# Kernel optimization log

Hardware: AMD Instinct MI355X
Metric: run time of the kernel (lower is better)

## Reference

```python
import jax, jax.numpy as jnp
import numpy as np

M, IN, H, OUT, B = 64, 64, 256, 1, 4096


def setup_inputs() -> dict:
    key = jax.random.key(0)
    ks = jax.random.split(key, 7)
    s1 = 1.0 / np.sqrt(IN)
    s2 = 1.0 / np.sqrt(H)
    return {
        "xs": jax.random.normal(ks[0], (M, B, IN), dtype=jnp.float32),
        "W1": jax.random.uniform(ks[1], (M, IN, H), minval=-s1, maxval=s1, dtype=jnp.float32),
        "b1": jax.random.uniform(ks[2], (M, H), minval=-s1, maxval=s1, dtype=jnp.float32),
        "W2": jax.random.uniform(ks[3], (M, H, H), minval=-s2, maxval=s2, dtype=jnp.float32),
        "b2": jax.random.uniform(ks[4], (M, H), minval=-s2, maxval=s2, dtype=jnp.float32),
        "W3": jax.random.uniform(ks[5], (M, H, OUT), minval=-s2, maxval=s2, dtype=jnp.float32),
        "b3": jax.random.uniform(ks[6], (M, OUT), minval=-s2, maxval=s2, dtype=jnp.float32),
    }


def reference(xs, W1, b1, W2, b2, W3, b3):
    # Batched over models: [M, B, in] x [M, in, h] -> [M, B, h]
    h1 = jax.nn.relu(jnp.einsum("mbi,mih->mbh", xs, W1) + b1[:, None, :])
    h2 = jax.nn.relu(jnp.einsum("mbh,mhk->mbk", h1, W2) + b2[:, None, :])
    out = jnp.einsum("mbh,mho->mbo", h2, W3) + b3[:, None, :]
    return out  # [M, B, out]
```

## Files before the change

### kernel.cpp

```cpp
#include <hip/hip_runtime.h>
#include <hip/hip_bf16.h>

#define NMODELS 64
#define BBATCH  4096
#define IN_DIM  64
#define H_DIM   256

typedef __attribute__((ext_vector_type(8))) short short8;
typedef __attribute__((ext_vector_type(4))) float floatx4;
typedef __attribute__((ext_vector_type(4))) unsigned int uint4v;
typedef __attribute__((ext_vector_type(2))) unsigned int uint2v;

__device__ __forceinline__ unsigned short f2bf(float f) {
    unsigned int u = __builtin_bit_cast(unsigned int, f);
    return (unsigned short)((u + 0x8000u) >> 16);
}
__device__ __forceinline__ unsigned int pkbf(float a, float b) {
    __hip_bfloat162 h = __float22bfloat162_rn(make_float2(a, b));
    unsigned int u;
    __builtin_memcpy(&u, &h, 4);
    return u;
}

__global__ __launch_bounds__(256) void prep_weights(const float* __restrict__ W1,
                                                    const float* __restrict__ W2,
                                                    unsigned short* __restrict__ w1t,
                                                    unsigned short* __restrict__ w2t) {
    __shared__ float lds[64][65];
    const int bid = blockIdx.x;
    const float* src;
    unsigned short* dst;
    int K, N, m, kb, nb;
    if (bid < 256) {
        m = bid >> 2; kb = 0; nb = bid & 3; K = IN_DIM; N = H_DIM;
        src = W1; dst = w1t;
    } else {
        int t = bid - 256;
        m = t >> 4; kb = (t >> 2) & 3; nb = t & 3; K = H_DIM; N = H_DIM;
        src = W2; dst = w2t;
    }
    const float* s = src + ((size_t)m * K + (size_t)kb * 64) * N + nb * 64;
    const int tid = threadIdx.x;
    const int r = tid >> 4, c4 = (tid & 15) * 4;
#pragma unroll
    for (int p = 0; p < 4; ++p) {
        int row = p * 16 + r;
        float4 v = *(const float4*)(s + (size_t)row * N + c4);
        lds[row][c4] = v.x; lds[row][c4 + 1] = v.y;
        lds[row][c4 + 2] = v.z; lds[row][c4 + 3] = v.w;
    }
    __syncthreads();
    unsigned short* dbase = dst + ((size_t)m * N + (size_t)nb * 64) * K + kb * 64;
    const int j = tid & 7;
#pragma unroll
    for (int it = 0; it < 2; ++it) {
        int n = it * 32 + (tid >> 3);
        unsigned short tmp[8];
#pragma unroll
        for (int e = 0; e < 8; ++e) tmp[e] = f2bf(lds[j * 8 + e][n]);
        *(short8*)(dbase + (size_t)n * K + j * 8) = *(const short8*)tmp;
    }
}

__global__ __launch_bounds__(256, 2) void mlp_fused(
    const float* __restrict__ xs,
    const unsigned short* __restrict__ w1t,
    const float* __restrict__ b1,
    const unsigned short* __restrict__ w2t,
    const float* __restrict__ b2,
    const float* __restrict__ w3,
    const float* __restrict__ b3,
    float* __restrict__ out)
{
    __shared__ unsigned short h1s[2][64 * 256];
    float* red = (float*)h1s;

    const int bid = blockIdx.x;
    const int m     = bid >> 5;
    const int tile0 = (bid & 31) * 2;
    const int tid = threadIdx.x;
    const int w   = tid >> 6;
    const int lane = tid & 63;
    const int q   = lane >> 4;
    const int c16 = lane & 15;
    const int sw  = c16 & 7;

    floatx4 b1v = *(const floatx4*)(b1 + m * H_DIM + w * 64 + c16 * 4);
    floatx4 b2v = *(const floatx4*)(b2 + m * H_DIM + w * 64 + c16 * 4);
    floatx4 w3v = *(const floatx4*)(w3 + m * H_DIM + w * 64 + c16 * 4);
    const float b3v = b3[m];

    const float* xrow0 = xs + ((size_t)m * BBATCH + (size_t)tile0 * 64) * IN_DIM;
    const unsigned short* w1p = w1t + (size_t)m * (H_DIM * IN_DIM)
                                + (w * 64 + c16 * 4) * IN_DIM + q * 8;
    const unsigned short* w2p = w2t + (size_t)m * (H_DIM * H_DIM)
                                + (w * 64 + c16 * 4) * H_DIM + q * 8;

    short8 ax[2][4][2];
#pragma unroll
    for (int t = 0; t < 2; ++t)
#pragma unroll
        for (int rb = 0; rb < 4; ++rb)
#pragma unroll
            for (int kb = 0; kb < 2; ++kb) {
                const float* xp = xrow0 + (size_t)t * 64 * IN_DIM
                                  + (rb * 16 + c16) * IN_DIM + kb * 32 + q * 8;
                float4 v0 = *(const float4*)xp;
                float4 v1 = *(const float4*)(xp + 4);
                uint4v u;
                u[0] = pkbf(v0.x, v0.y); u[1] = pkbf(v0.z, v0.w);
                u[2] = pkbf(v1.x, v1.y); u[3] = pkbf(v1.z, v1.w);
                ax[t][rb][kb] = __builtin_bit_cast(short8, u);
            }

    floatx4 acc[2][4][4];
#pragma unroll
    for (int t = 0; t < 2; ++t)
#pragma unroll
        for (int rb = 0; rb < 4; ++rb)
#pragma unroll
            for (int nb = 0; nb < 4; ++nb)
                acc[t][rb][nb] = (floatx4){0.f, 0.f, 0.f, 0.f};

    {
        short8 bw[2][4];
#pragma unroll
        for (int kb = 0; kb < 2; ++kb)
#pragma unroll
            for (int nb = 0; nb < 4; ++nb)
                bw[kb][nb] = *(const short8*)(w1p + nb * IN_DIM + kb * 32);
#pragma unroll
        for (int t = 0; t < 2; ++t)
#pragma unroll
            for (int kb = 0; kb < 2; ++kb)
#pragma unroll
                for (int nb = 0; nb < 4; ++nb)
#pragma unroll
                    for (int rb = 0; rb < 4; ++rb)
                        acc[t][rb][nb] = __builtin_amdgcn_mfma_f32_16x16x32_bf16(
                            ax[t][rb][kb], bw[kb][nb], acc[t][rb][nb], 0, 0, 0);
    }

    short8 bv[3][4];
#pragma unroll
    for (int nb = 0; nb < 4; ++nb) bv[0][nb] = *(const short8*)(w2p + nb * H_DIM + 0 * 32);
#pragma unroll
    for (int nb = 0; nb < 4; ++nb) bv[1][nb] = *(const short8*)(w2p + nb * H_DIM + 1 * 32);

    {
#pragma unroll
        for (int t = 0; t < 2; ++t)
#pragma unroll
            for (int rb = 0; rb < 4; ++rb)
#pragma unroll
                for (int r = 0; r < 4; ++r) {
                    float v0 = fmaxf(acc[t][rb][0][r] + b1v[0], 0.f);
                    float v1 = fmaxf(acc[t][rb][1][r] + b1v[1], 0.f);
                    float v2 = fmaxf(acc[t][rb][2][r] + b1v[2], 0.f);
                    float v3 = fmaxf(acc[t][rb][3][r] + b1v[3], 0.f);
                    uint2v u; u[0] = pkbf(v0, v1); u[1] = pkbf(v2, v3);
                    int row = rb * 16 + q * 4 + r;
                    int chunk = (w * 8 + (c16 >> 1)) ^ (row & 7);
                    *(uint2v*)((char*)&h1s[t][0] + row * 512 + chunk * 16 + (c16 & 1) * 8) = u;
                }
    }
    __syncthreads();

#pragma unroll
    for (int t = 0; t < 2; ++t)
#pragma unroll
        for (int rb = 0; rb < 4; ++rb)
#pragma unroll
            for (int nb = 0; nb < 4; ++nb)
                acc[t][rb][nb] = (floatx4){0.f, 0.f, 0.f, 0.f};

#pragma unroll
    for (int kb = 0; kb < 8; ++kb) {
        const int cur = kb % 3;
        const int pre = (kb + 2) % 3;
        if (kb < 6) {
#pragma unroll
            for (int nb = 0; nb < 4; ++nb)
                bv[pre][nb] = *(const short8*)(w2p + nb * H_DIM + (kb + 2) * 32);
        }
        short8 av[2][4];
#pragma unroll
        for (int t = 0; t < 2; ++t)
#pragma unroll
            for (int rb = 0; rb < 4; ++rb)
                av[t][rb] = *(const short8*)((char*)&h1s[t][0] + (rb * 16 + c16) * 512
                                             + (((kb * 4 + q) ^ sw) * 16));
#pragma unroll
        for (int nb = 0; nb < 4; ++nb)
#pragma unroll
            for (int t = 0; t < 2; ++t)
#pragma unroll
                for (int rb = 0; rb < 4; ++rb)
                    acc[t][rb][nb] = __builtin_amdgcn_mfma_f32_16x16x32_bf16(
                        av[t][rb], bv[cur][nb], acc[t][rb][nb], 0, 0, 0);
    }

    float p[2][4][4];
#pragma unroll
    for (int t = 0; t < 2; ++t)
#pragma unroll
        for (int rb = 0; rb < 4; ++rb)
#pragma unroll
            for (int r = 0; r < 4; ++r) p[t][rb][r] = 0.f;
#pragma unroll
    for (int t = 0; t < 2; ++t)
#pragma unroll
        for (int rb = 0; rb < 4; ++rb)
#pragma unroll
            for (int nb = 0; nb < 4; ++nb)
#pragma unroll
                for (int r = 0; r < 4; ++r) {
                    float v = fmaxf(acc[t][rb][nb][r] + b2v[nb], 0.f);
                    p[t][rb][r] += v * w3v[nb];
                }
#pragma unroll
    for (int off = 1; off < 16; off <<= 1)
#pragma unroll
        for (int t = 0; t < 2; ++t)
#pragma unroll
            for (int rb = 0; rb < 4; ++rb)
#pragma unroll
                for (int r = 0; r < 4; ++r)
                    p[t][rb][r] += __shfl_xor(p[t][rb][r], off);

    __syncthreads();
    if (c16 == 0) {
#pragma unroll
        for (int t = 0; t < 2; ++t)
#pragma unroll
            for (int rb = 0; rb < 4; ++rb)
#pragma unroll
                for (int r = 0; r < 4; ++r)
                    red[t * 256 + w * 64 + rb * 16 + q * 4 + r] = p[t][rb][r];
    }
    __syncthreads();
    if (tid < 128) {
        int t = tid >> 6, rr = tid & 63;
        const float* rt = red + t * 256;
        float s = rt[rr] + rt[64 + rr] + rt[128 + rr] + rt[192 + rr] + b3v;
        out[(size_t)m * BBATCH + (tile0 + t) * 64 + rr] = s;
    }
}

extern "C" void kernel_launch(void* const* d_in, const int* in_sizes, int n_in,
                              void* d_out, int out_size, void* d_ws, size_t ws_size,
                              hipStream_t stream) {
    const float* xs = (const float*)d_in[0];
    const float* W1 = (const float*)d_in[1];
    const float* b1 = (const float*)d_in[2];
    const float* W2 = (const float*)d_in[3];
    const float* b2 = (const float*)d_in[4];
    const float* W3 = (const float*)d_in[5];
    const float* b3 = (const float*)d_in[6];
    float* out = (float*)d_out;

    unsigned short* w1t = (unsigned short*)d_ws;
    unsigned short* w2t = w1t + (size_t)NMODELS * H_DIM * IN_DIM;

    prep_weights<<<256 + NMODELS * 16, 256, 0, stream>>>(W1, W2, w1t, w2t);
    mlp_fused<<<NMODELS * (BBATCH / 128), 256, 0, stream>>>(xs, w1t, b1, w2t, b2, W3, b3, out);
}
```

Measured before the change: 181.2 us.

## Process one 64-row tile per block to raise occupancy

Each block now handles a single 64-row batch tile instead of two. This halves the LDS buffer, the accumulator registers and the A-fragment registers, so launch bounds can ask for three blocks per CU and the grid doubles. The W2 prefetch pipeline also shrinks from triple to double buffering. The trade-off is that each W2 fragment loaded from global or L2 is reused across half as many rows, which doubles weight traffic per output.

```diff
diff --git a/kernel.cpp b/kernel.cpp
--- a/kernel.cpp
+++ b/kernel.cpp
@@ -62,7 +62,7 @@
     }
 }
 
-__global__ __launch_bounds__(256, 2) void mlp_fused(
+__global__ __launch_bounds__(256, 3) void mlp_fused(
     const float* __restrict__ xs,
     const unsigned short* __restrict__ w1t,
     const float* __restrict__ b1,
@@ -72,55 +72,50 @@
     const float* __restrict__ b3,
     float* __restrict__ out)
 {
-    __shared__ unsigned short h1s[2][64 * 256];
-    float* red = (float*)h1s;
-
-    const int bid = blockIdx.x;
-    const int m     = bid >> 5;
-    const int tile0 = (bid & 31) * 2;
-    const int tid = threadIdx.x;
-    const int w   = tid >> 6;
+    __shared__ unsigned short h1s[64 * 256];
+    float* red = (float*)&h1s[0];
+
+    const int bid  = blockIdx.x;
+    const int m    = bid >> 6;
+    const int tile = bid & 63;
+    const int tid  = threadIdx.x;
+    const int w    = tid >> 6;
     const int lane = tid & 63;
-    const int q   = lane >> 4;
-    const int c16 = lane & 15;
-    const int sw  = c16 & 7;
+    const int q    = lane >> 4;
+    const int c16  = lane & 15;
+    const int sw   = c16 & 7;
 
     floatx4 b1v = *(const floatx4*)(b1 + m * H_DIM + w * 64 + c16 * 4);
     floatx4 b2v = *(const floatx4*)(b2 + m * H_DIM + w * 64 + c16 * 4);
     floatx4 w3v = *(const floatx4*)(w3 + m * H_DIM + w * 64 + c16 * 4);
     const float b3v = b3[m];
 
-    const float* xrow0 = xs + ((size_t)m * BBATCH + (size_t)tile0 * 64) * IN_DIM;
+    const float* xrow0 = xs + ((size_t)m * BBATCH + (size_t)tile * 64) * IN_DIM;
     const unsigned short* w1p = w1t + (size_t)m * (H_DIM * IN_DIM)
                                 + (w * 64 + c16 * 4) * IN_DIM + q * 8;
     const unsigned short* w2p = w2t + (size_t)m * (H_DIM * H_DIM)
                                 + (w * 64 + c16 * 4) * H_DIM + q * 8;
 
-    short8 ax[2][4][2];
-#pragma unroll
-    for (int t = 0; t < 2; ++t)
-#pragma unroll
-        for (int rb = 0; rb < 4; ++rb)
-#pragma unroll
-            for (int kb = 0; kb < 2; ++kb) {
-                const float* xp = xrow0 + (size_t)t * 64 * IN_DIM
-                                  + (rb * 16 + c16) * IN_DIM + kb * 32 + q * 8;
-                float4 v0 = *(const float4*)xp;
-                float4 v1 = *(const float4*)(xp + 4);
-                uint4v u;
-                u[0] = pkbf(v0.x, v0.y); u[1] = pkbf(v0.z, v0.w);
-                u[2] = pkbf(v1.x, v1.y); u[3] = pkbf(v1.z, v1.w);
-                ax[t][rb][kb] = __builtin_bit_cast(short8, u);
-            }
-
-    floatx4 acc[2][4][4];
-#pragma unroll
-    for (int t = 0; t < 2; ++t)
-#pragma unroll
-        for (int rb = 0; rb < 4; ++rb)
-#pragma unroll
-            for (int nb = 0; nb < 4; ++nb)
-                acc[t][rb][nb] = (floatx4){0.f, 0.f, 0.f, 0.f};
+    short8 ax[4][2];
+#pragma unroll
+    for (int rb = 0; rb < 4; ++rb)
+#pragma unroll
+        for (int kb = 0; kb < 2; ++kb) {
+            const float* xp = xrow0 + (rb * 16 + c16) * IN_DIM + kb * 32 + q * 8;
+            float4 v0 = *(const float4*)xp;
+            float4 v1 = *(const float4*)(xp + 4);
+            uint4v u;
+            u[0] = pkbf(v0.x, v0.y); u[1] = pkbf(v0.z, v0.w);
+            u[2] = pkbf(v1.x, v1.y); u[3] = pkbf(v1.z, v1.w);
+            ax[rb][kb] = __builtin_bit_cast(short8, u);
+        }
+
+    floatx4 acc[4][4];
+#pragma unroll
+    for (int rb = 0; rb < 4; ++rb)
+#pragma unroll
+        for (int nb = 0; nb < 4; ++nb)
+            acc[rb][nb] = (floatx4){0.f, 0.f, 0.f, 0.f};
 
     {
         short8 bw[2][4];
@@ -130,120 +125,97 @@
             for (int nb = 0; nb < 4; ++nb)
                 bw[kb][nb] = *(const short8*)(w1p + nb * IN_DIM + kb * 32);
 #pragma unroll
-        for (int t = 0; t < 2; ++t)
-#pragma unroll
-            for (int kb = 0; kb < 2; ++kb)
-#pragma unroll
-                for (int nb = 0; nb < 4; ++nb)
-#pragma unroll
-                    for (int rb = 0; rb < 4; ++rb)
-                        acc[t][rb][nb] = __builtin_amdgcn_mfma_f32_16x16x32_bf16(
-                            ax[t][rb][kb], bw[kb][nb], acc[t][rb][nb], 0, 0, 0);
-    }
-
-    short8 bv[3][4];
-#pragma unroll
-    for (int nb = 0; nb < 4; ++nb) bv[0][nb] = *(const short8*)(w2p + nb * H_DIM + 0 * 32);
-#pragma unroll
-    for (int nb = 0; nb < 4; ++nb) bv[1][nb] = *(const short8*)(w2p + nb * H_DIM + 1 * 32);
+        for (int kb = 0; kb < 2; ++kb)
+#pragma unroll
+            for (int nb = 0; nb < 4; ++nb)
+#pragma unroll
+                for (int rb = 0; rb < 4; ++rb)
+                    acc[rb][nb] = __builtin_amdgcn_mfma_f32_16x16x32_bf16(
+                        ax[rb][kb], bw[kb][nb], acc[rb][nb], 0, 0, 0);
+    }
+
+    short8 bv[2][4];
+#pragma unroll
+    for (int nb = 0; nb < 4; ++nb)
+        bv[0][nb] = *(const short8*)(w2p + nb * H_DIM);
 
     {
 #pragma unroll
-        for (int t = 0; t < 2; ++t)
+        for (int rb = 0; rb < 4; ++rb)
+#pragma unroll
+            for (int r = 0; r < 4; ++r) {
+                float v0 = fmaxf(acc[rb][0][r] + b1v[0], 0.f);
+                float v1 = fmaxf(acc[rb][1][r] + b1v[1], 0.f);
+                float v2 = fmaxf(acc[rb][2][r] + b1v[2], 0.f);
+                float v3 = fmaxf(acc[rb][3][r] + b1v[3], 0.f);
+                uint2v u2; u2[0] = pkbf(v0, v1); u2[1] = pkbf(v2, v3);
+                int row = rb * 16 + q * 4 + r;
+                int chunk = (w * 8 + (c16 >> 1)) ^ (row & 7);
+                *(uint2v*)((char*)&h1s[0] + row * 512 + chunk * 16 + (c16 & 1) * 8) = u2;
+            }
+    }
+    __syncthreads();
+
+#pragma unroll
+    for (int rb = 0; rb < 4; ++rb)
+#pragma unroll
+        for (int nb = 0; nb < 4; ++nb)
+            acc[rb][nb] = (floatx4){0.f, 0.f, 0.f, 0.f};
+
+#pragma unroll
+    for (int kb = 0; kb < 8; ++kb) {
+        if (kb < 7) {
+#pragma unroll
+            for (int nb = 0; nb < 4; ++nb)
+                bv[(kb + 1) & 1][nb] = *(const short8*)(w2p + nb * H_DIM + (kb + 1) * 32);
+        }
+        short8 av[4];
+#pragma unroll
+        for (int rb = 0; rb < 4; ++rb)
+            av[rb] = *(const short8*)((char*)&h1s[0] + (rb * 16 + c16) * 512
+                                      + (((kb * 4 + q) ^ sw) * 16));
+#pragma unroll
+        for (int nb = 0; nb < 4; ++nb)
 #pragma unroll
             for (int rb = 0; rb < 4; ++rb)
-#pragma unroll
-                for (int r = 0; r < 4; ++r) {
-                    float v0 = fmaxf(acc[t][rb][0][r] + b1v[0], 0.f);
-                    float v1 = fmaxf(acc[t][rb][1][r] + b1v[1], 0.f);
-                    float v2 = fmaxf(acc[t][rb][2][r] + b1v[2], 0.f);
-                    float v3 = fmaxf(acc[t][rb][3][r] + b1v[3], 0.f);
-                    uint2v u; u[0] = pkbf(v0, v1); u[1] = pkbf(v2, v3);
-                    int row = rb * 16 + q * 4 + r;
-                    int chunk = (w * 8 + (c16 >> 1)) ^ (row & 7);
-                    *(uint2v*)((char*)&h1s[t][0] + row * 512 + chunk * 16 + (c16 & 1) * 8) = u;
-                }
-    }
-    __syncthreads();
-
-#pragma unroll
-    for (int t = 0; t < 2; ++t)
-#pragma unroll
-        for (int rb = 0; rb < 4; ++rb)
-#pragma unroll
-            for (int nb = 0; nb < 4; ++nb)
-                acc[t][rb][nb] = (floatx4){0.f, 0.f, 0.f, 0.f};
-
-#pragma unroll
-    for (int kb = 0; kb < 8; ++kb) {
-        const int cur = kb % 3;
-        const int pre = (kb + 2) % 3;
-        if (kb < 6) {
-#pragma unroll
-            for (int nb = 0; nb < 4; ++nb)
-                bv[pre][nb] = *(const short8*)(w2p + nb * H_DIM + (kb + 2) * 32);
-        }
-        short8 av[2][4];
-#pragma unroll
-        for (int t = 0; t < 2; ++t)
-#pragma unroll
-            for (int rb = 0; rb < 4; ++rb)
-                av[t][rb] = *(const short8*)((char*)&h1s[t][0] + (rb * 16 + c16) * 512
-                                             + (((kb * 4 + q) ^ sw) * 16));
-#pragma unroll
-        for (int nb = 0; nb < 4; ++nb)
-#pragma unroll
-            for (int t = 0; t < 2; ++t)
-#pragma unroll
-                for (int rb = 0; rb < 4; ++rb)
-                    acc[t][rb][nb] = __builtin_amdgcn_mfma_f32_16x16x32_bf16(
-                        av[t][rb], bv[cur][nb], acc[t][rb][nb], 0, 0, 0);
-    }
-
-    float p[2][4][4];
-#pragma unroll
-    for (int t = 0; t < 2; ++t)
-#pragma unroll
-        for (int rb = 0; rb < 4; ++rb)
-#pragma unroll
-            for (int r = 0; r < 4; ++r) p[t][rb][r] = 0.f;
-#pragma unroll
-    for (int t = 0; t < 2; ++t)
-#pragma unroll
-        for (int rb = 0; rb < 4; ++rb)
-#pragma unroll
-            for (int nb = 0; nb < 4; ++nb)
-#pragma unroll
-                for (int r = 0; r < 4; ++r) {
-                    float v = fmaxf(acc[t][rb][nb][r] + b2v[nb], 0.f);
-                    p[t][rb][r] += v * w3v[nb];
-                }
+                acc[rb][nb] = __builtin_amdgcn_mfma_f32_16x16x32_bf16(
+                    av[rb], bv[kb & 1][nb], acc[rb][nb], 0, 0, 0);
+    }
+
+    float p[4][4];
+#pragma unroll
+    for (int rb = 0; rb < 4; ++rb)
+#pragma unroll
+        for (int r = 0; r < 4; ++r) p[rb][r] = 0.f;
+#pragma unroll
+    for (int rb = 0; rb < 4; ++rb)
+#pragma unroll
+        for (int nb = 0; nb < 4; ++nb)
+#pragma unroll
+            for (int r = 0; r < 4; ++r) {
+                float v = fmaxf(acc[rb][nb][r] + b2v[nb], 0.f);
+                p[rb][r] += v * w3v[nb];
+            }
 #pragma unroll
     for (int off = 1; off < 16; off <<= 1)
 #pragma unroll
-        for (int t = 0; t < 2; ++t)
-#pragma unroll
-            for (int rb = 0; rb < 4; ++rb)
-#pragma unroll
-                for (int r = 0; r < 4; ++r)
-                    p[t][rb][r] += __shfl_xor(p[t][rb][r], off);
+        for (int rb = 0; rb < 4; ++rb)
+#pragma unroll
+            for (int r = 0; r < 4; ++r)
+                p[rb][r] += __shfl_xor(p[rb][r], off);
 
     __syncthreads();
     if (c16 == 0) {
 #pragma unroll
-        for (int t = 0; t < 2; ++t)
-#pragma unroll
-            for (int rb = 0; rb < 4; ++rb)
-#pragma unroll
-                for (int r = 0; r < 4; ++r)
-                    red[t * 256 + w * 64 + rb * 16 + q * 4 + r] = p[t][rb][r];
-    }
-    __syncthreads();
-    if (tid < 128) {
-        int t = tid >> 6, rr = tid & 63;
-        const float* rt = red + t * 256;
-        float s = rt[rr] + rt[64 + rr] + rt[128 + rr] + rt[192 + rr] + b3v;
-        out[(size_t)m * BBATCH + (tile0 + t) * 64 + rr] = s;
+        for (int rb = 0; rb < 4; ++rb)
+#pragma unroll
+            for (int r = 0; r < 4; ++r)
+                red[w * 64 + rb * 16 + q * 4 + r] = p[rb][r];
+    }
+    __syncthreads();
+    if (tid < 64) {
+        float s = red[tid] + red[64 + tid] + red[128 + tid] + red[192 + tid] + b3v;
+        out[(size_t)m * BBATCH + tile * 64 + tid] = s;
     }
 }
 
@@ -263,5 +235,5 @@
     unsigned short* w2t = w1t + (size_t)NMODELS * H_DIM * IN_DIM;
 
     prep_weights<<<256 + NMODELS * 16, 256, 0, stream>>>(W1, W2, w1t, w2t);
-    mlp_fused<<<NMODELS * (BBATCH / 128), 256, 0, stream>>>(xs, w1t, b1, w2t, b2, W3, b3, out);
-}
+    mlp_fused<<<NMODELS * (BBATCH / 64), 256, 0, stream>>>(xs, w1t, b1, w2t, b2, W3, b3, out);
+}
```

After: 215.3 us. 18.8% more time.

## Make fused MLP blocks persistent over four tiles and prefetch next x tile

Applied to the files above, without the earlier changes.

Shrinks the grid from 2048 to 512 blocks, each looping over four 128-row tiles of one model. The next tile's input rows are prefetched into registers during the layer-2 MFMA loop and the output reduction, hiding global load latency. Each block also reuses the same model's biases and weights across tiles. The trade-off is more live registers, an extra barrier per iteration, and fewer blocks to fill the device (512 blocks on 256 CUs at 2 per CU).

```diff
diff --git a/kernel.cpp b/kernel.cpp
--- a/kernel.cpp
+++ b/kernel.cpp
@@ -62,6 +62,31 @@
     }
 }
 
+__device__ __forceinline__ void loadx(const float* __restrict__ xp0, int c16, int q,
+                                      float4 (&xr)[4][2][2]) {
+#pragma unroll
+    for (int rb = 0; rb < 4; ++rb)
+#pragma unroll
+        for (int kb = 0; kb < 2; ++kb) {
+            const float* xp = xp0 + (rb * 16 + c16) * IN_DIM + kb * 32 + q * 8;
+            xr[rb][kb][0] = *(const float4*)xp;
+            xr[rb][kb][1] = *(const float4*)(xp + 4);
+        }
+}
+
+__device__ __forceinline__ void cvtx(const float4 (&xr)[4][2][2], short8 (&axd)[4][2]) {
+#pragma unroll
+    for (int rb = 0; rb < 4; ++rb)
+#pragma unroll
+        for (int kb = 0; kb < 2; ++kb) {
+            const float4 v0 = xr[rb][kb][0], v1 = xr[rb][kb][1];
+            uint4v u;
+            u[0] = pkbf(v0.x, v0.y); u[1] = pkbf(v0.z, v0.w);
+            u[2] = pkbf(v1.x, v1.y); u[3] = pkbf(v1.z, v1.w);
+            axd[rb][kb] = __builtin_bit_cast(short8, u);
+        }
+}
+
 __global__ __launch_bounds__(256, 2) void mlp_fused(
     const float* __restrict__ xs,
     const unsigned short* __restrict__ w1t,
@@ -73,177 +98,187 @@
     float* __restrict__ out)
 {
     __shared__ unsigned short h1s[2][64 * 256];
-    float* red = (float*)h1s;
-
-    const int bid = blockIdx.x;
-    const int m     = bid >> 5;
-    const int tile0 = (bid & 31) * 2;
-    const int tid = threadIdx.x;
-    const int w   = tid >> 6;
+    float* red = (float*)&h1s[0][0];
+
+    const int p      = blockIdx.x;
+    const int m      = p >> 3;
+    const int tpbase = (p & 7) * 4;
+    const int tid  = threadIdx.x;
+    const int w    = tid >> 6;
     const int lane = tid & 63;
-    const int q   = lane >> 4;
-    const int c16 = lane & 15;
-    const int sw  = c16 & 7;
+    const int q    = lane >> 4;
+    const int c16  = lane & 15;
+    const int sw   = c16 & 7;
 
     floatx4 b1v = *(const floatx4*)(b1 + m * H_DIM + w * 64 + c16 * 4);
     floatx4 b2v = *(const floatx4*)(b2 + m * H_DIM + w * 64 + c16 * 4);
     floatx4 w3v = *(const floatx4*)(w3 + m * H_DIM + w * 64 + c16 * 4);
     const float b3v = b3[m];
 
-    const float* xrow0 = xs + ((size_t)m * BBATCH + (size_t)tile0 * 64) * IN_DIM;
     const unsigned short* w1p = w1t + (size_t)m * (H_DIM * IN_DIM)
                                 + (w * 64 + c16 * 4) * IN_DIM + q * 8;
     const unsigned short* w2p = w2t + (size_t)m * (H_DIM * H_DIM)
                                 + (w * 64 + c16 * 4) * H_DIM + q * 8;
-
+    const float* xbase = xs + (size_t)m * BBATCH * IN_DIM;
+
+    float4 xr[4][2][2];
     short8 ax[2][4][2];
-#pragma unroll
-    for (int t = 0; t < 2; ++t)
-#pragma unroll
-        for (int rb = 0; rb < 4; ++rb)
-#pragma unroll
-            for (int kb = 0; kb < 2; ++kb) {
-                const float* xp = xrow0 + (size_t)t * 64 * IN_DIM
-                                  + (rb * 16 + c16) * IN_DIM + kb * 32 + q * 8;
-                float4 v0 = *(const float4*)xp;
-                float4 v1 = *(const float4*)(xp + 4);
-                uint4v u;
-                u[0] = pkbf(v0.x, v0.y); u[1] = pkbf(v0.z, v0.w);
-                u[2] = pkbf(v1.x, v1.y); u[3] = pkbf(v1.z, v1.w);
-                ax[t][rb][kb] = __builtin_bit_cast(short8, u);
+
+    {
+        const float* x0 = xbase + (size_t)(tpbase * 128) * IN_DIM;
+        loadx(x0, c16, q, xr);
+        cvtx(xr, ax[0]);
+        loadx(x0 + 64 * IN_DIM, c16, q, xr);
+    }
+
+    floatx4 acc[2][4][4];
+    short8 bv[3][4];
+
+#pragma unroll 1
+    for (int i = 0; i < 4; ++i) {
+        cvtx(xr, ax[1]);
+
+#pragma unroll
+        for (int t = 0; t < 2; ++t)
+#pragma unroll
+            for (int rb = 0; rb < 4; ++rb)
+#pragma unroll
+                for (int nb = 0; nb < 4; ++nb)
+                    acc[t][rb][nb] = (floatx4){0.f, 0.f, 0.f, 0.f};
+        {
+            short8 bw[2][4];
+#pragma unroll
+            for (int kb = 0; kb < 2; ++kb)
+#pragma unroll
+                for (int nb = 0; nb < 4; ++nb)
+                    bw[kb][nb] = *(const short8*)(w1p + nb * IN_DIM + kb * 32);
+#pragma unroll
+            for (int t = 0; t < 2; ++t)
+#pragma unroll
+                for (int kb = 0; kb < 2; ++kb)
+#pragma unroll
+                    for (int nb = 0; nb < 4; ++nb)
+#pragma unroll
+                        for (int rb = 0; rb < 4; ++rb)
+                            acc[t][rb][nb] = __builtin_amdgcn_mfma_f32_16x16x32_bf16(
+                                ax[t][rb][kb], bw[kb][nb], acc[t][rb][nb], 0, 0, 0);
+        }
+
+#pragma unroll
+        for (int nb = 0; nb < 4; ++nb) bv[0][nb] = *(const short8*)(w2p + nb * H_DIM + 0 * 32);
+#pragma unroll
+        for (int nb = 0; nb < 4; ++nb) bv[1][nb] = *(const short8*)(w2p + nb * H_DIM + 1 * 32);
+
+        {
+#pragma unroll
+            for (int t = 0; t < 2; ++t)
+#pragma unroll
+                for (int rb = 0; rb < 4; ++rb)
+#pragma unroll
+                    for (int r = 0; r < 4; ++r) {
+                        float v0 = fmaxf(acc[t][rb][0][r] + b1v[0], 0.f);
+                        float v1 = fmaxf(acc[t][rb][1][r] + b1v[1], 0.f);
+                        float v2 = fmaxf(acc[t][rb][2][r] + b1v[2], 0.f);
+                        float v3 = fmaxf(acc[t][rb][3][r] + b1v[3], 0.f);
+                        uint2v u2; u2[0] = pkbf(v0, v1); u2[1] = pkbf(v2, v3);
+                        int row = rb * 16 + q * 4 + r;
+                        int chunk = (w * 8 + (c16 >> 1)) ^ (row & 7);
+                        *(uint2v*)((char*)&h1s[t][0] + row * 512 + chunk * 16 + (c16 & 1) * 8) = u2;
+                    }
+        }
+        __syncthreads();
+
+#pragma unroll
+        for (int t = 0; t < 2; ++t)
+#pragma unroll
+            for (int rb = 0; rb < 4; ++rb)
+#pragma unroll
+                for (int nb = 0; nb < 4; ++nb)
+                    acc[t][rb][nb] = (floatx4){0.f, 0.f, 0.f, 0.f};
+
+#pragma unroll
+        for (int kb = 0; kb < 8; ++kb) {
+            const int cur = kb % 3;
+            const int pre = (kb + 2) % 3;
+            if (kb < 6) {
+#pragma unroll
+                for (int nb = 0; nb < 4; ++nb)
+                    bv[pre][nb] = *(const short8*)(w2p + nb * H_DIM + (kb + 2) * 32);
             }
-
-    floatx4 acc[2][4][4];
-#pragma unroll
-    for (int t = 0; t < 2; ++t)
-#pragma unroll
-        for (int rb = 0; rb < 4; ++rb)
+            if (kb == 6 && i < 3) {
+                const float* xn = xbase + (size_t)((tpbase + i + 1) * 128) * IN_DIM;
+                loadx(xn, c16, q, xr);
+            }
+            short8 av[2][4];
+#pragma unroll
+            for (int t = 0; t < 2; ++t)
+#pragma unroll
+                for (int rb = 0; rb < 4; ++rb)
+                    av[t][rb] = *(const short8*)((char*)&h1s[t][0] + (rb * 16 + c16) * 512
+                                                 + (((kb * 4 + q) ^ sw) * 16));
 #pragma unroll
             for (int nb = 0; nb < 4; ++nb)
-                acc[t][rb][nb] = (floatx4){0.f, 0.f, 0.f, 0.f};
-
-    {
-        short8 bw[2][4];
-#pragma unroll
-        for (int kb = 0; kb < 2; ++kb)
-#pragma unroll
-            for (int nb = 0; nb < 4; ++nb)
-                bw[kb][nb] = *(const short8*)(w1p + nb * IN_DIM + kb * 32);
-#pragma unroll
-        for (int t = 0; t < 2; ++t)
-#pragma unroll
-            for (int kb = 0; kb < 2; ++kb)
-#pragma unroll
-                for (int nb = 0; nb < 4; ++nb)
+#pragma unroll
+                for (int t = 0; t < 2; ++t)
 #pragma unroll
                     for (int rb = 0; rb < 4; ++rb)
                         acc[t][rb][nb] = __builtin_amdgcn_mfma_f32_16x16x32_bf16(
-                            ax[t][rb][kb], bw[kb][nb], acc[t][rb][nb], 0, 0, 0);
-    }
-
-    short8 bv[3][4];
-#pragma unroll
-    for (int nb = 0; nb < 4; ++nb) bv[0][nb] = *(const short8*)(w2p + nb * H_DIM + 0 * 32);
-#pragma unroll
-    for (int nb = 0; nb < 4; ++nb) bv[1][nb] = *(const short8*)(w2p + nb * H_DIM + 1 * 32);
-
-    {
+                            av[t][rb], bv[cur][nb], acc[t][rb][nb], 0, 0, 0);
+        }
+
+        float pp[2][4][4];
 #pragma unroll
         for (int t = 0; t < 2; ++t)
 #pragma unroll
             for (int rb = 0; rb < 4; ++rb)
 #pragma unroll
-                for (int r = 0; r < 4; ++r) {
-                    float v0 = fmaxf(acc[t][rb][0][r] + b1v[0], 0.f);
-                    float v1 = fmaxf(acc[t][rb][1][r] + b1v[1], 0.f);
-                    float v2 = fmaxf(acc[t][rb][2][r] + b1v[2], 0.f);
-                    float v3 = fmaxf(acc[t][rb][3][r] + b1v[3], 0.f);
-                    uint2v u; u[0] = pkbf(v0, v1); u[1] = pkbf(v2, v3);
-                    int row = rb * 16 + q * 4 + r;
-                    int chunk = (w * 8 + (c16 >> 1)) ^ (row & 7);
-                    *(uint2v*)((char*)&h1s[t][0] + row * 512 + chunk * 16 + (c16 & 1) * 8) = u;
-                }
-    }
-    __syncthreads();
-
-#pragma unroll
-    for (int t = 0; t < 2; ++t)
-#pragma unroll
-        for (int rb = 0; rb < 4; ++rb)
-#pragma unroll
-            for (int nb = 0; nb < 4; ++nb)
-                acc[t][rb][nb] = (floatx4){0.f, 0.f, 0.f, 0.f};
-
-#pragma unroll
-    for (int kb = 0; kb < 8; ++kb) {
-        const int cur = kb % 3;
-        const int pre = (kb + 2) % 3;
-        if (kb < 6) {
-#pragma unroll
-            for (int nb = 0; nb < 4; ++nb)
-                bv[pre][nb] = *(const short8*)(w2p + nb * H_DIM + (kb + 2) * 32);
-        }
-        short8 av[2][4];
+                for (int r = 0; r < 4; ++r) pp[t][rb][r] = 0.f;
 #pragma unroll
         for (int t = 0; t < 2; ++t)
 #pragma unroll
             for (int rb = 0; rb < 4; ++rb)
-                av[t][rb] = *(const short8*)((char*)&h1s[t][0] + (rb * 16 + c16) * 512
-                                             + (((kb * 4 + q) ^ sw) * 16));
-#pragma unroll
-        for (int nb = 0; nb < 4; ++nb)
+#pragma unroll
+                for (int nb = 0; nb < 4; ++nb)
+#pragma unroll
+                    for (int r = 0; r < 4; ++r) {
+                        float v = fmaxf(acc[t][rb][nb][r] + b2v[nb], 0.f);
+                        pp[t][rb][r] += v * w3v[nb];
+                    }
+
+        if (i < 3) {
+            cvtx(xr, ax[0]);
+            const float* xn = xbase + (size_t)((tpbase + i + 1) * 128) * IN_DIM;
+            loadx(xn + 64 * IN_DIM, c16, q, xr);
+        }
+
+#pragma unroll
+        for (int off = 1; off < 16; off <<= 1)
 #pragma unroll
             for (int t = 0; t < 2; ++t)
 #pragma unroll
                 for (int rb = 0; rb < 4; ++rb)
-                    acc[t][rb][nb] = __builtin_amdgcn_mfma_f32_16x16x32_bf16(
-                        av[t][rb], bv[cur][nb], acc[t][rb][nb], 0, 0, 0);
-    }
-
-    float p[2][4][4];
-#pragma unroll
-    for (int t = 0; t < 2; ++t)
-#pragma unroll
-        for (int rb = 0; rb < 4; ++rb)
-#pragma unroll
-            for (int r = 0; r < 4; ++r) p[t][rb][r] = 0.f;
-#pragma unroll
-    for (int t = 0; t < 2; ++t)
-#pragma unroll
-        for (int rb = 0; rb < 4; ++rb)
-#pragma unroll
-            for (int nb = 0; nb < 4; ++nb)
-#pragma unroll
-                for (int r = 0; r < 4; ++r) {
-                    float v = fmaxf(acc[t][rb][nb][r] + b2v[nb], 0.f);
-                    p[t][rb][r] += v * w3v[nb];
-                }
-#pragma unroll
-    for (int off = 1; off < 16; off <<= 1)
-#pragma unroll
-        for (int t = 0; t < 2; ++t)
-#pragma unroll
-            for (int rb = 0; rb < 4; ++rb)
-#pragma unroll
-                for (int r = 0; r < 4; ++r)
-                    p[t][rb][r] += __shfl_xor(p[t][rb][r], off);
-
-    __syncthreads();
-    if (c16 == 0) {
-#pragma unroll
-        for (int t = 0; t < 2; ++t)
-#pragma unroll
-            for (int rb = 0; rb < 4; ++rb)
-#pragma unroll
-                for (int r = 0; r < 4; ++r)
-                    red[t * 256 + w * 64 + rb * 16 + q * 4 + r] = p[t][rb][r];
-    }
-    __syncthreads();
-    if (tid < 128) {
-        int t = tid >> 6, rr = tid & 63;
-        const float* rt = red + t * 256;
-        float s = rt[rr] + rt[64 + rr] + rt[128 + rr] + rt[192 + rr] + b3v;
-        out[(size_t)m * BBATCH + (tile0 + t) * 64 + rr] = s;
+#pragma unroll
+                    for (int r = 0; r < 4; ++r)
+                        pp[t][rb][r] += __shfl_xor(pp[t][rb][r], off);
+
+        __syncthreads();
+        if (c16 == 0) {
+#pragma unroll
+            for (int t = 0; t < 2; ++t)
+#pragma unroll
+                for (int rb = 0; rb < 4; ++rb)
+#pragma unroll
+                    for (int r = 0; r < 4; ++r)
+                        red[t * 256 + w * 64 + rb * 16 + q * 4 + r] = pp[t][rb][r];
+        }
+        __syncthreads();
+        if (tid < 128) {
+            int t = tid >> 6, rr = tid & 63;
+            const float* rt = red + t * 256;
+            float s = rt[rr] + rt[64 + rr] + rt[128 + rr] + rt[192 + rr] + b3v;
+            out[(size_t)m * BBATCH + (tpbase + i) * 128 + tid] = s;
+        }
+        __syncthreads();
     }
 }
 
@@ -263,5 +298,5 @@
     unsigned short* w2t = w1t + (size_t)NMODELS * H_DIM * IN_DIM;
 
     prep_weights<<<256 + NMODELS * 16, 256, 0, stream>>>(W1, W2, w1t, w2t);
-    mlp_fused<<<NMODELS * (BBATCH / 128), 256, 0, stream>>>(xs, w1t, b1, w2t, b2, W3, b3, out);
-}
+    mlp_fused<<<NMODELS * 8, 256, 0, stream>>>(xs, w1t, b1, w2t, b2, W3, b3, out);
+}
```

Result: slower. 280.6 us (+54.8%).
